# Kernel tuning notes

Measured on AMD Instinct MI355X. Metric: run time of the kernel, lower is better.

## Reference

```python
import jax, jax.numpy as jnp
import numpy as np

N_Q = 16
N_K = 16
D_QK = 64
D_V = 64
# torch module default scale=1.0 saturates softmax at feature width 1024;
# we use the conventional sqrt(d) scale for well-conditioned numerics.
SCALE = 32.0  # sqrt(N_Q * D_QK)
DROPOUT_P = 0.0  # dropout is identity at p=0


def setup_inputs() -> dict:
    key = jax.random.key(0)
    kq, kk, kv = jax.random.split(key, 3)
    S = 8192
    return {
        "query": jax.random.normal(kq, (S, N_Q, D_QK), dtype=jnp.float32),
        "key": jax.random.normal(kk, (S, N_K, D_QK), dtype=jnp.float32),
        "value": jax.random.normal(kv, (S, N_K, D_V), dtype=jnp.float32),
    }


def reference(query, key, value):
    # Flatten trailing (head, dim) into one feature axis, as the torch view does.
    q = query.reshape(-1, N_Q * D_QK)            # [S_q, 1024]
    k = key.reshape(-1, N_K * D_QK)              # [S_k, 1024]
    v = value.reshape(-1, N_K * D_V)             # [S_k, 1024]
    scores = jnp.matmul(q, k.T) / SCALE          # [S_q, S_k]
    attn = jax.nn.softmax(scores, axis=-1)       # dropout_p=0 -> identity
    out = jnp.matmul(attn, v)                    # [S_q, 1024]
    return out.reshape(query.shape[:-1] + (-1,))  # [S_q, N_Q, D_V]
```

## Files before the change

### kernel.cpp

```cpp
#include <hip/hip_runtime.h>
#include <hip/hip_bf16.h>


typedef __bf16 bf16x8 __attribute__((ext_vector_type(8)));
typedef float f32x4 __attribute__((ext_vector_type(4)));
typedef const __attribute__((address_space(1))) unsigned int* as1p;
typedef __attribute__((address_space(3))) unsigned int* as3p;
typedef unsigned short u16;

__device__ __forceinline__ u16 f2bf(float x) {
  unsigned u = __float_as_uint(x);
  u += 0x7fffu + ((u >> 16) & 1u);
  return (u16)(u >> 16);
}
__device__ __forceinline__ float bf2f(u16 b) { return __uint_as_float(((unsigned)b) << 16); }
__device__ __forceinline__ unsigned pack2(float lo, float hi) {
  return (unsigned)f2bf(lo) | ((unsigned)f2bf(hi) << 16);
}

#define BAR()   do { __builtin_amdgcn_s_barrier(); asm volatile("" ::: "memory"); } while (0)
#define LGKM0() do { asm volatile("s_waitcnt lgkmcnt(0)" ::: "memory"); __builtin_amdgcn_sched_barrier(0); } while (0)
#define VM(n)   do { asm volatile("s_waitcnt vmcnt(" #n ")" ::: "memory"); __builtin_amdgcn_sched_barrier(0); } while (0)

__global__ __launch_bounds__(256) void cvt_bf16(const float* __restrict__ in,
                                                unsigned short* __restrict__ out) {
  const size_t i = (size_t)blockIdx.x * 256 + threadIdx.x;
  const float4* p = (const float4*)in + i * 2;
  float4 a = p[0], b = p[1];
  uint4 o;
  o.x = pack2(a.x, a.y);
  o.y = pack2(a.z, a.w);
  o.z = pack2(b.x, b.y);
  o.w = pack2(b.z, b.w);
  ((uint4*)out)[i] = o;
}

__global__ __launch_bounds__(256) void transpose_bf16(const float* __restrict__ V,
                                                      unsigned short* __restrict__ VT) {
  __shared__ float t[64][65];
  const int rb = blockIdx.x * 64;
  const int cb = blockIdx.y * 64;
  const int tid = threadIdx.x;
#pragma unroll
  for (int it = 0; it < 4; ++it) {
    int r = it * 16 + (tid >> 4);
    int c = (tid & 15) * 4;
    float4 x = *(const float4*)(V + (size_t)(rb + r) * 1024 + cb + c);
    t[r][c] = x.x; t[r][c + 1] = x.y; t[r][c + 2] = x.z; t[r][c + 3] = x.w;
  }
  __syncthreads();
  const int j = tid & 63;
  const int c0 = (tid >> 6) * 16;
#pragma unroll
  for (int i = 0; i < 16; ++i) {
    int c = c0 + i;
    VT[(size_t)(cb + c) * 8192 + rb + j] = f2bf(t[j][c]);
  }
}

template <int BM, int OUTMODE, int DEC>
__global__ __launch_bounds__(512, 2) void gemm8(const u16* __restrict__ A,
                                                const u16* __restrict__ B,
                                                void* __restrict__ Cv,
                                                const float* __restrict__ inv,
                                                float* __restrict__ partials,
                                                int K, int ldc, float scale) {
  constexpr int MF = BM / 32;
  constexpr int MH = MF / 2;
  constexpr int LA = BM / 64;
  constexpr int NU = (LA + 4) / 2;
  constexpr int ABUF = BM * 128;
  constexpr int BBUF = 32768;
  constexpr int BUFSZ = ABUF + BBUF;
  static_assert(NU == 3 || NU == 4, "");
  __shared__ __align__(1024) char smem[2 * BUFSZ];

  const int tid = threadIdx.x;
  const int lane = tid & 63, wave = tid >> 6;
  const int wr = wave >> 2, wc = wave & 3;
  const int lan15 = lane & 15, g = lane >> 4, l7 = lane & 7;

  const int nwg = gridDim.x;
  const int wg = (blockIdx.x & 7) * (nwg >> 3) + (blockIdx.x >> 3);

  int bm0, bn0;
  if constexpr (DEC == 0) {
    const int r = wg & 255;
    bm0 = (r >> 3) * 256;
    bn0 = (((wg >> 8) << 3) | (r & 7)) * 256;
  } else {
    bm0 = (wg & 63) * BM;
    bn0 = (wg >> 6) * 256;
  }

  const int sr = tid >> 3;
  const int scb = ((tid & 7) ^ (sr & 7)) * 8;
  const u16* Ags = A + (size_t)(bm0 + sr) * K + scb;
  const u16* Bgs = B + (size_t)(bn0 + sr) * K + scb;

  const int sa0 = ((0 + g) ^ l7) * 16;
  const int sa1 = ((4 + g) ^ l7) * 16;
  const int abase = (wr * (BM / 2) + lan15) * 128;
  const int bbase = ABUF + (wc * 64 + lan15) * 128;

  f32x4 acc[MF][4];
#pragma unroll
  for (int m = 0; m < MF; ++m)
#pragma unroll
    for (int n = 0; n < 4; ++n) acc[m][n] = f32x4{0.f, 0.f, 0.f, 0.f};

  const int nt = K >> 6;
  const int niter = nt >> 1;

  auto ISSUE_UNIT = [&](int t, int u) {
    const int bb = (t & 1) * BUFSZ;
    const size_t ko = (size_t)t * 64;
    if (2 * u < LA) {
#pragma unroll
      for (int s = 0; s < 2; ++s) {
        const int j = 2 * u + s;
        __builtin_amdgcn_global_load_lds((as1p)(Ags + (size_t)j * 64 * K + ko),
                                         (as3p)(smem + bb + j * 8192 + tid * 16), 16, 0, 0);
      }
    } else {
#pragma unroll
      for (int s = 0; s < 2; ++s) {
        const int j = 2 * u - LA + s;
        __builtin_amdgcn_global_load_lds((as1p)(Bgs + (size_t)j * 64 * K + ko),
                                         (as3p)(smem + bb + ABUF + j * 8192 + tid * 16), 16, 0, 0);
      }
    }
  };

  bf16x8 a[MH][2], b[4][2];
  auto DS_A = [&](int bb, int mh) {
#pragma unroll
    for (int m = 0; m < MH; ++m) {
      a[m][0] = *(const bf16x8*)(smem + bb + abase + (mh * MH + m) * 2048 + sa0);
      a[m][1] = *(const bf16x8*)(smem + bb + abase + (mh * MH + m) * 2048 + sa1);
    }
  };
  auto DS_B = [&](int bb, int nh) {
#pragma unroll
    for (int n = 0; n < 2; ++n) {
      b[nh * 2 + n][0] = *(const bf16x8*)(smem + bb + bbase + (nh * 2 + n) * 2048 + sa0);
      b[nh * 2 + n][1] = *(const bf16x8*)(smem + bb + bbase + (nh * 2 + n) * 2048 + sa1);
    }
  };
  auto MMA = [&](int mh, int nh) {
    __builtin_amdgcn_s_setprio(1);
#pragma unroll
    for (int m = 0; m < MH; ++m)
#pragma unroll
      for (int n = 0; n < 2; ++n)
#pragma unroll
        for (int ks = 0; ks < 2; ++ks)
          acc[mh * MH + m][nh * 2 + n] = __builtin_amdgcn_mfma_f32_16x16x32_bf16(
              a[m][ks], b[nh * 2 + n][ks], acc[mh * MH + m][nh * 2 + n], 0, 0, 0);
    __builtin_amdgcn_s_setprio(0);
  };

#pragma unroll
  for (int u = 0; u < NU; ++u) ISSUE_UNIT(0, u);
  ISSUE_UNIT(1, 0);
  VM(2);
  BAR();

  for (int i = 0; i < niter; ++i) {
    const int t0 = 2 * i;
    const bool more = (i + 1 < niter);

    DS_A(0, 0); DS_B(0, 0);
    ISSUE_UNIT(t0 + 1, 1);
    BAR(); MMA(0, 0); BAR();

    DS_B(0, 1);
    if constexpr (NU >= 3) ISSUE_UNIT(t0 + 1, 2);
    BAR(); MMA(0, 1); BAR();

    DS_A(0, 1);
    if constexpr (NU >= 4) ISSUE_UNIT(t0 + 1, 3);
    BAR(); MMA(1, 0); LGKM0(); BAR();

    if (more) ISSUE_UNIT(t0 + 2, 0);
    BAR(); MMA(1, 1);
    if (more) { VM(2); } else { VM(0); }
    BAR();

    DS_A(BUFSZ, 0); DS_B(BUFSZ, 0);
    if (more) ISSUE_UNIT(t0 + 2, 1);
    BAR(); MMA(0, 0); BAR();

    DS_B(BUFSZ, 1);
    if (more) { if constexpr (NU >= 3) ISSUE_UNIT(t0 + 2, 2); }
    BAR(); MMA(0, 1); BAR();

    DS_A(BUFSZ, 1);
    if (more) { if constexpr (NU >= 4) ISSUE_UNIT(t0 + 2, 3); }
    BAR(); MMA(1, 0); LGKM0(); BAR();

    if (more) ISSUE_UNIT(t0 + 3, 0);
    BAR(); MMA(1, 1);
    if (more) { VM(2); } else { VM(0); }
    BAR();
  }

  const int c0 = bn0 + wc * 64 + lan15;
  if constexpr (OUTMODE == 0) {
    u16* C = (u16*)Cv;
    const int cb4 = (bn0 >> 8) * 4 + wc;
#pragma unroll
    for (int m = 0; m < MF; ++m)
#pragma unroll
      for (int r = 0; r < 4; ++r) {
        const int row = bm0 + wr * (BM / 2) + m * 16 + g * 4 + r;
        float part = 0.f;
#pragma unroll
        for (int n = 0; n < 4; ++n) {
          float v = __expf(acc[m][n][r] * scale);
          C[(size_t)row * ldc + c0 + n * 16] = f2bf(v);
          part += v;
        }
        part += __shfl_xor(part, 1, 64);
        part += __shfl_xor(part, 2, 64);
        part += __shfl_xor(part, 4, 64);
        part += __shfl_xor(part, 8, 64);
        if (lan15 == 0) partials[(size_t)row * 128 + cb4] = part;
      }
  } else {
    float* C = (float*)Cv;
#pragma unroll
    for (int m = 0; m < MF; ++m)
#pragma unroll
      for (int r = 0; r < 4; ++r) {
        const int row = bm0 + wr * (BM / 2) + m * 16 + g * 4 + r;
        const float iv = inv ? inv[row] : 1.0f;
#pragma unroll
        for (int n = 0; n < 4; ++n)
          C[(size_t)row * ldc + c0 + n * 16] = acc[m][n][r] * iv;
      }
  }
}

__global__ __launch_bounds__(256) void rowinv(const float* __restrict__ partials,
                                              float* __restrict__ inv) {
  const int row = blockIdx.x * 256 + threadIdx.x;
  const float4* p = (const float4*)(partials + (size_t)row * 128);
  float s = 0.f;
#pragma unroll
  for (int j = 0; j < 32; ++j) {
    float4 v = p[j];
    s += (v.x + v.y) + (v.z + v.w);
  }
  inv[row] = 1.0f / s;
}

__global__ __launch_bounds__(256) void normalize_inplace(u16* __restrict__ E) {
  __shared__ float red[4];
  u16* row = E + (size_t)blockIdx.x * 8192;
  const int tid = threadIdx.x;
  float f[32];
  float s = 0.f;
#pragma unroll
  for (int c = 0; c < 4; ++c) {
    uint4 v = *((const uint4*)row + c * 256 + tid);
    unsigned u[4] = {v.x, v.y, v.z, v.w};
#pragma unroll
    for (int q = 0; q < 4; ++q) {
      f[c * 8 + q * 2] = bf2f((u16)(u[q] & 0xffffu));
      f[c * 8 + q * 2 + 1] = bf2f((u16)(u[q] >> 16));
      s += f[c * 8 + q * 2] + f[c * 8 + q * 2 + 1];
    }
  }
#pragma unroll
  for (int off = 32; off; off >>= 1) s += __shfl_xor(s, off, 64);
  if ((tid & 63) == 0) red[tid >> 6] = s;
  __syncthreads();
  const float iv = 1.0f / ((red[0] + red[1]) + (red[2] + red[3]));
#pragma unroll
  for (int c = 0; c < 4; ++c) {
    uint4 o;
    o.x = pack2(f[c * 8 + 0] * iv, f[c * 8 + 1] * iv);
    o.y = pack2(f[c * 8 + 2] * iv, f[c * 8 + 3] * iv);
    o.z = pack2(f[c * 8 + 4] * iv, f[c * 8 + 5] * iv);
    o.w = pack2(f[c * 8 + 6] * iv, f[c * 8 + 7] * iv);
    *((uint4*)row + c * 256 + tid) = o;
  }
}

extern "C" void kernel_launch(void* const* d_in, const int* in_sizes, int n_in,
                              void* d_out, int out_size, void* d_ws, size_t ws_size,
                              hipStream_t stream) {
  const float* Q = (const float*)d_in[0];
  const float* K = (const float*)d_in[1];
  const float* V = (const float*)d_in[2];

  char* ws = (char*)d_ws;
  u16* S = (u16*)ws;
  u16* VT = (u16*)(ws + (size_t)134217728);
  float* partials = (float*)(ws + (size_t)134217728 + 16777216);
  float* inv = (float*)(ws + (size_t)134217728 + 16777216 + 4194304);
  const bool haveInv =
      ws_size >= (size_t)134217728 + 16777216 + 4194304 + 32768;

  u16* Qb = (u16*)d_out;
  u16* Kb = Qb + 8388608;

  cvt_bf16<<<4096, 256, 0, stream>>>(Q, Qb);
  cvt_bf16<<<4096, 256, 0, stream>>>(K, Kb);
  transpose_bf16<<<dim3(128, 16), 256, 0, stream>>>(V, VT);

  gemm8<256, 0, 0><<<1024, 512, 0, stream>>>(
      Qb, Kb, S, nullptr, haveInv ? partials : (float*)(ws + 134217728 + 16777216),
      1024, 8192, 1.0f / 32.0f);

  if (haveInv) {
    rowinv<<<32, 256, 0, stream>>>(partials, inv);
    gemm8<128, 1, 1><<<256, 512, 0, stream>>>(
        S, VT, d_out, inv, nullptr, 8192, 1024, 1.0f);
  } else {
    normalize_inplace<<<8192, 256, 0, stream>>>(S);
    gemm8<128, 1, 1><<<256, 512, 0, stream>>>(
        S, VT, d_out, nullptr, nullptr, 8192, 1024, 1.0f);
  }
}
```

Before: 305.6 us.

## Replace 8-phase interleaved GEMM schedule with simple per-tile double-buffered loop

The main loop of both GEMM kernels changes from an 8-phase schedule that interleaved LDS reads, split global-to-LDS load units and MFMA groups with many barriers into a simpler loop. Each K-tile now loads all A/B fragments, runs all MFMAs, syncs once, then issues the whole tile two ahead. This removes most barriers and the fine-grained load splitting. In exchange the LDS-read latency is no longer hidden behind MFMA work, and more fragments are held in registers at once, which raises register pressure.

```diff
diff --git a/kernel.cpp b/kernel.cpp
--- a/kernel.cpp
+++ b/kernel.cpp
@@ -59,20 +59,20 @@
 }
 
 template <int BM, int OUTMODE, int DEC>
-__global__ __launch_bounds__(512, 2) void gemm8(const u16* __restrict__ A,
-                                                const u16* __restrict__ B,
-                                                void* __restrict__ Cv,
-                                                const float* __restrict__ inv,
-                                                float* __restrict__ partials,
-                                                int K, int ldc, float scale) {
+__global__ __launch_bounds__(512, 2) void gemm_fr(const u16* __restrict__ A,
+                                                  const u16* __restrict__ B,
+                                                  void* __restrict__ Cv,
+                                                  const float* __restrict__ inv,
+                                                  float* __restrict__ partials,
+                                                  int K, int ldc, float scale) {
   constexpr int MF = BM / 32;
   constexpr int MH = MF / 2;
   constexpr int LA = BM / 64;
-  constexpr int NU = (LA + 4) / 2;
+  constexpr int LB = 4;
+  constexpr int LPT = LA + LB;
   constexpr int ABUF = BM * 128;
   constexpr int BBUF = 32768;
   constexpr int BUFSZ = ABUF + BBUF;
-  static_assert(NU == 3 || NU == 4, "");
   __shared__ __align__(1024) char smem[2 * BUFSZ];
 
   const int tid = threadIdx.x;
@@ -110,98 +110,88 @@
     for (int n = 0; n < 4; ++n) acc[m][n] = f32x4{0.f, 0.f, 0.f, 0.f};
 
   const int nt = K >> 6;
-  const int niter = nt >> 1;
-
-  auto ISSUE_UNIT = [&](int t, int u) {
+
+  auto ISSUE = [&](int t) {
     const int bb = (t & 1) * BUFSZ;
     const size_t ko = (size_t)t * 64;
-    if (2 * u < LA) {
-#pragma unroll
-      for (int s = 0; s < 2; ++s) {
-        const int j = 2 * u + s;
-        __builtin_amdgcn_global_load_lds((as1p)(Ags + (size_t)j * 64 * K + ko),
-                                         (as3p)(smem + bb + j * 8192 + tid * 16), 16, 0, 0);
+#pragma unroll
+    for (int j = 0; j < LA; ++j)
+      __builtin_amdgcn_global_load_lds((as1p)(Ags + (size_t)j * 64 * K + ko),
+                                       (as3p)(smem + bb + j * 8192 + tid * 16), 16, 0, 0);
+#pragma unroll
+    for (int j = 0; j < LB; ++j)
+      __builtin_amdgcn_global_load_lds((as1p)(Bgs + (size_t)j * 64 * K + ko),
+                                       (as3p)(smem + bb + ABUF + j * 8192 + tid * 16), 16, 0, 0);
+  };
+
+  ISSUE(0);
+  ISSUE(1);
+  if constexpr (LPT == 8) { VM(8); } else { VM(6); }
+  BAR();
+
+  for (int t = 0; t < nt; ++t) {
+    const char* bp = smem + (t & 1) * BUFSZ;
+
+    bf16x8 a0[MH][2], b0[4][2], a1[MH][2];
+#pragma unroll
+    for (int m = 0; m < MH; ++m) {
+      a0[m][0] = *(const bf16x8*)(bp + abase + m * 2048 + sa0);
+      a0[m][1] = *(const bf16x8*)(bp + abase + m * 2048 + sa1);
+    }
+#pragma unroll
+    for (int n = 0; n < 4; ++n) {
+      b0[n][0] = *(const bf16x8*)(bp + bbase + n * 2048 + sa0);
+      b0[n][1] = *(const bf16x8*)(bp + bbase + n * 2048 + sa1);
+    }
+#pragma unroll
+    for (int m = 0; m < MH; ++m) {
+      a1[m][0] = *(const bf16x8*)(bp + abase + (MH + m) * 2048 + sa0);
+      a1[m][1] = *(const bf16x8*)(bp + abase + (MH + m) * 2048 + sa1);
+    }
+
+    __builtin_amdgcn_s_setprio(1);
+#pragma unroll
+    for (int m = 0; m < MH; ++m)
+#pragma unroll
+      for (int n = 0; n < 2; ++n)
+#pragma unroll
+        for (int ks = 0; ks < 2; ++ks)
+          acc[m][n] = __builtin_amdgcn_mfma_f32_16x16x32_bf16(a0[m][ks], b0[n][ks], acc[m][n], 0, 0, 0);
+#pragma unroll
+    for (int m = 0; m < MH; ++m)
+#pragma unroll
+      for (int n = 0; n < 2; ++n)
+#pragma unroll
+        for (int ks = 0; ks < 2; ++ks)
+          acc[m][2 + n] = __builtin_amdgcn_mfma_f32_16x16x32_bf16(a0[m][ks], b0[2 + n][ks], acc[m][2 + n], 0, 0, 0);
+#pragma unroll
+    for (int m = 0; m < MH; ++m)
+#pragma unroll
+      for (int n = 0; n < 2; ++n)
+#pragma unroll
+        for (int ks = 0; ks < 2; ++ks)
+          acc[MH + m][n] = __builtin_amdgcn_mfma_f32_16x16x32_bf16(a1[m][ks], b0[n][ks], acc[MH + m][n], 0, 0, 0);
+#pragma unroll
+    for (int m = 0; m < MH; ++m)
+#pragma unroll
+      for (int n = 0; n < 2; ++n)
+#pragma unroll
+        for (int ks = 0; ks < 2; ++ks)
+          acc[MH + m][2 + n] = __builtin_amdgcn_mfma_f32_16x16x32_bf16(a1[m][ks], b0[2 + n][ks], acc[MH + m][2 + n], 0, 0, 0);
+    __builtin_amdgcn_s_setprio(0);
+
+    LGKM0();
+    BAR();
+
+    const bool st = (t + 2 < nt);
+    if (st) ISSUE(t + 2);
+    if (t + 1 < nt) {
+      if (st) {
+        if constexpr (LPT == 8) { VM(8); } else { VM(6); }
+      } else {
+        VM(0);
       }
-    } else {
-#pragma unroll
-      for (int s = 0; s < 2; ++s) {
-        const int j = 2 * u - LA + s;
-        __builtin_amdgcn_global_load_lds((as1p)(Bgs + (size_t)j * 64 * K + ko),
-                                         (as3p)(smem + bb + ABUF + j * 8192 + tid * 16), 16, 0, 0);
-      }
-    }
-  };
-
-  bf16x8 a[MH][2], b[4][2];
-  auto DS_A = [&](int bb, int mh) {
-#pragma unroll
-    for (int m = 0; m < MH; ++m) {
-      a[m][0] = *(const bf16x8*)(smem + bb + abase + (mh * MH + m) * 2048 + sa0);
-      a[m][1] = *(const bf16x8*)(smem + bb + abase + (mh * MH + m) * 2048 + sa1);
-    }
-  };
-  auto DS_B = [&](int bb, int nh) {
-#pragma unroll
-    for (int n = 0; n < 2; ++n) {
-      b[nh * 2 + n][0] = *(const bf16x8*)(smem + bb + bbase + (nh * 2 + n) * 2048 + sa0);
-      b[nh * 2 + n][1] = *(const bf16x8*)(smem + bb + bbase + (nh * 2 + n) * 2048 + sa1);
-    }
-  };
-  auto MMA = [&](int mh, int nh) {
-    __builtin_amdgcn_s_setprio(1);
-#pragma unroll
-    for (int m = 0; m < MH; ++m)
-#pragma unroll
-      for (int n = 0; n < 2; ++n)
-#pragma unroll
-        for (int ks = 0; ks < 2; ++ks)
-          acc[mh * MH + m][nh * 2 + n] = __builtin_amdgcn_mfma_f32_16x16x32_bf16(
-              a[m][ks], b[nh * 2 + n][ks], acc[mh * MH + m][nh * 2 + n], 0, 0, 0);
-    __builtin_amdgcn_s_setprio(0);
-  };
-
-#pragma unroll
-  for (int u = 0; u < NU; ++u) ISSUE_UNIT(0, u);
-  ISSUE_UNIT(1, 0);
-  VM(2);
-  BAR();
-
-  for (int i = 0; i < niter; ++i) {
-    const int t0 = 2 * i;
-    const bool more = (i + 1 < niter);
-
-    DS_A(0, 0); DS_B(0, 0);
-    ISSUE_UNIT(t0 + 1, 1);
-    BAR(); MMA(0, 0); BAR();
-
-    DS_B(0, 1);
-    if constexpr (NU >= 3) ISSUE_UNIT(t0 + 1, 2);
-    BAR(); MMA(0, 1); BAR();
-
-    DS_A(0, 1);
-    if constexpr (NU >= 4) ISSUE_UNIT(t0 + 1, 3);
-    BAR(); MMA(1, 0); LGKM0(); BAR();
-
-    if (more) ISSUE_UNIT(t0 + 2, 0);
-    BAR(); MMA(1, 1);
-    if (more) { VM(2); } else { VM(0); }
-    BAR();
-
-    DS_A(BUFSZ, 0); DS_B(BUFSZ, 0);
-    if (more) ISSUE_UNIT(t0 + 2, 1);
-    BAR(); MMA(0, 0); BAR();
-
-    DS_B(BUFSZ, 1);
-    if (more) { if constexpr (NU >= 3) ISSUE_UNIT(t0 + 2, 2); }
-    BAR(); MMA(0, 1); BAR();
-
-    DS_A(BUFSZ, 1);
-    if (more) { if constexpr (NU >= 4) ISSUE_UNIT(t0 + 2, 3); }
-    BAR(); MMA(1, 0); LGKM0(); BAR();
-
-    if (more) ISSUE_UNIT(t0 + 3, 0);
-    BAR(); MMA(1, 1);
-    if (more) { VM(2); } else { VM(0); }
+    }
     BAR();
   }
 
@@ -310,17 +300,17 @@
   cvt_bf16<<<4096, 256, 0, stream>>>(K, Kb);
   transpose_bf16<<<dim3(128, 16), 256, 0, stream>>>(V, VT);
 
-  gemm8<256, 0, 0><<<1024, 512, 0, stream>>>(
+  gemm_fr<256, 0, 0><<<1024, 512, 0, stream>>>(
       Qb, Kb, S, nullptr, haveInv ? partials : (float*)(ws + 134217728 + 16777216),
       1024, 8192, 1.0f / 32.0f);
 
   if (haveInv) {
     rowinv<<<32, 256, 0, stream>>>(partials, inv);
-    gemm8<128, 1, 1><<<256, 512, 0, stream>>>(
+    gemm_fr<128, 1, 1><<<256, 512, 0, stream>>>(
         S, VT, d_out, inv, nullptr, 8192, 1024, 1.0f);
   } else {
     normalize_inplace<<<8192, 256, 0, stream>>>(S);
-    gemm8<128, 1, 1><<<256, 512, 0, stream>>>(
+    gemm_fr<128, 1, 1><<<256, 512, 0, stream>>>(
         S, VT, d_out, nullptr, nullptr, 8192, 1024, 1.0f);
   }
 }
```

New measurement: 320.7 us. 4.9% more time.

## Reorder GEMM prefetch schedule for deeper lookahead and remap second-GEMM tile order

Applied to the files above, without the earlier changes.

Global-to-LDS loads are now issued at a finer granularity and in a new order. Each half of the next A/B tiles is prefetched as soon as the matching LDS sub-buffer has been read, which deepens the outstanding loads (vmcnt 6 or 4 instead of 2). LDS-read waits are placed before each MMA phase rather than only before the third. Separately, the second GEMM's workgroup-to-tile mapping groups 8 M-blocks by all 4 N-blocks, so neighbouring blocks share S rows and VT columns in cache. The risks are buffer-reuse hazards from the earlier overwrites and extra lgkm stalls.

```diff
diff --git a/kernel.cpp b/kernel.cpp
--- a/kernel.cpp
+++ b/kernel.cpp
@@ -59,20 +59,17 @@
 }
 
 template <int BM, int OUTMODE, int DEC>
-__global__ __launch_bounds__(512, 2) void gemm8(const u16* __restrict__ A,
-                                                const u16* __restrict__ B,
-                                                void* __restrict__ Cv,
-                                                const float* __restrict__ inv,
-                                                float* __restrict__ partials,
-                                                int K, int ldc, float scale) {
+__global__ __launch_bounds__(512, 2) void gemm8d(const u16* __restrict__ A,
+                                                 const u16* __restrict__ B,
+                                                 void* __restrict__ Cv,
+                                                 const float* __restrict__ inv,
+                                                 float* __restrict__ partials,
+                                                 int K, int ldc, float scale) {
   constexpr int MF = BM / 32;
   constexpr int MH = MF / 2;
-  constexpr int LA = BM / 64;
-  constexpr int NU = (LA + 4) / 2;
   constexpr int ABUF = BM * 128;
   constexpr int BBUF = 32768;
   constexpr int BUFSZ = ABUF + BBUF;
-  static_assert(NU == 3 || NU == 4, "");
   __shared__ __align__(1024) char smem[2 * BUFSZ];
 
   const int tid = threadIdx.x;
@@ -82,15 +79,16 @@
 
   const int nwg = gridDim.x;
   const int wg = (blockIdx.x & 7) * (nwg >> 3) + (blockIdx.x >> 3);
-
   int bm0, bn0;
   if constexpr (DEC == 0) {
     const int r = wg & 255;
     bm0 = (r >> 3) * 256;
     bn0 = (((wg >> 8) << 3) | (r & 7)) * 256;
   } else {
-    bm0 = (wg & 63) * BM;
-    bn0 = (wg >> 6) * 256;
+    const int chunk = wg >> 5;
+    const int within = wg & 31;
+    bm0 = (chunk * 8 + (within >> 2)) * BM;
+    bn0 = (within & 3) * 256;
   }
 
   const int sr = tid >> 3;
@@ -112,25 +110,24 @@
   const int nt = K >> 6;
   const int niter = nt >> 1;
 
-  auto ISSUE_UNIT = [&](int t, int u) {
-    const int bb = (t & 1) * BUFSZ;
+  auto IA = [&](int t, int ja, int jb) {
+    char* bb = smem + (t & 1) * BUFSZ;
     const size_t ko = (size_t)t * 64;
-    if (2 * u < LA) {
-#pragma unroll
-      for (int s = 0; s < 2; ++s) {
-        const int j = 2 * u + s;
-        __builtin_amdgcn_global_load_lds((as1p)(Ags + (size_t)j * 64 * K + ko),
-                                         (as3p)(smem + bb + j * 8192 + tid * 16), 16, 0, 0);
-      }
-    } else {
-#pragma unroll
-      for (int s = 0; s < 2; ++s) {
-        const int j = 2 * u - LA + s;
-        __builtin_amdgcn_global_load_lds((as1p)(Bgs + (size_t)j * 64 * K + ko),
-                                         (as3p)(smem + bb + ABUF + j * 8192 + tid * 16), 16, 0, 0);
-      }
-    }
-  };
+    __builtin_amdgcn_global_load_lds((as1p)(Ags + (size_t)ja * 64 * K + ko),
+                                     (as3p)(bb + ja * 8192 + tid * 16), 16, 0, 0);
+    __builtin_amdgcn_global_load_lds((as1p)(Ags + (size_t)jb * 64 * K + ko),
+                                     (as3p)(bb + jb * 8192 + tid * 16), 16, 0, 0);
+  };
+  auto IB = [&](int t, int j0) {
+    char* bb = smem + (t & 1) * BUFSZ + ABUF;
+    const size_t ko = (size_t)t * 64;
+    __builtin_amdgcn_global_load_lds((as1p)(Bgs + (size_t)j0 * 64 * K + ko),
+                                     (as3p)(bb + j0 * 8192 + tid * 16), 16, 0, 0);
+    __builtin_amdgcn_global_load_lds((as1p)(Bgs + (size_t)(j0 + 1) * 64 * K + ko),
+                                     (as3p)(bb + (j0 + 1) * 8192 + tid * 16), 16, 0, 0);
+  };
+  auto IA_mh0 = [&](int t) { if constexpr (BM == 256) IA(t, 0, 2); };
+  auto IA_mh1 = [&](int t) { if constexpr (BM == 256) IA(t, 1, 3); else IA(t, 0, 1); };
 
   bf16x8 a[MH][2], b[4][2];
   auto DS_A = [&](int bb, int mh) {
@@ -160,10 +157,15 @@
     __builtin_amdgcn_s_setprio(0);
   };
 
-#pragma unroll
-  for (int u = 0; u < NU; ++u) ISSUE_UNIT(0, u);
-  ISSUE_UNIT(1, 0);
-  VM(2);
+  if constexpr (BM == 256) {
+    IA(0, 0, 2); IB(0, 0); IB(0, 2); IA(0, 1, 3);
+    IA(1, 0, 2); IB(1, 0); IB(1, 2);
+    VM(6);
+  } else {
+    IB(0, 0); IB(0, 2); IA(0, 0, 1);
+    IB(1, 0); IB(1, 2);
+    VM(4);
+  }
   BAR();
 
   for (int i = 0; i < niter; ++i) {
@@ -171,37 +173,37 @@
     const bool more = (i + 1 < niter);
 
     DS_A(0, 0); DS_B(0, 0);
-    ISSUE_UNIT(t0 + 1, 1);
-    BAR(); MMA(0, 0); BAR();
+    IA_mh1(t0 + 1);
+    BAR(); LGKM0(); MMA(0, 0); BAR();
 
     DS_B(0, 1);
-    if constexpr (NU >= 3) ISSUE_UNIT(t0 + 1, 2);
-    BAR(); MMA(0, 1); BAR();
+    if (more) IA_mh0(t0 + 2);
+    BAR(); LGKM0(); MMA(0, 1); BAR();
 
     DS_A(0, 1);
-    if constexpr (NU >= 4) ISSUE_UNIT(t0 + 1, 3);
-    BAR(); MMA(1, 0); LGKM0(); BAR();
-
-    if (more) ISSUE_UNIT(t0 + 2, 0);
+    if (more) IB(t0 + 2, 0);
+    BAR(); LGKM0(); MMA(1, 0); BAR();
+
+    if (more) IB(t0 + 2, 2);
     BAR(); MMA(1, 1);
-    if (more) { VM(2); } else { VM(0); }
+    if (more) { if constexpr (BM == 256) VM(6); else VM(4); } else { VM(0); }
     BAR();
 
     DS_A(BUFSZ, 0); DS_B(BUFSZ, 0);
-    if (more) ISSUE_UNIT(t0 + 2, 1);
-    BAR(); MMA(0, 0); BAR();
+    if (more) IA_mh1(t0 + 2);
+    BAR(); LGKM0(); MMA(0, 0); BAR();
 
     DS_B(BUFSZ, 1);
-    if (more) { if constexpr (NU >= 3) ISSUE_UNIT(t0 + 2, 2); }
-    BAR(); MMA(0, 1); BAR();
+    if (more) IA_mh0(t0 + 3);
+    BAR(); LGKM0(); MMA(0, 1); BAR();
 
     DS_A(BUFSZ, 1);
-    if (more) { if constexpr (NU >= 4) ISSUE_UNIT(t0 + 2, 3); }
-    BAR(); MMA(1, 0); LGKM0(); BAR();
-
-    if (more) ISSUE_UNIT(t0 + 3, 0);
+    if (more) IB(t0 + 3, 0);
+    BAR(); LGKM0(); MMA(1, 0); BAR();
+
+    if (more) IB(t0 + 3, 2);
     BAR(); MMA(1, 1);
-    if (more) { VM(2); } else { VM(0); }
+    if (more) { if constexpr (BM == 256) VM(6); else VM(4); } else { VM(0); }
     BAR();
   }
 
@@ -310,17 +312,17 @@
   cvt_bf16<<<4096, 256, 0, stream>>>(K, Kb);
   transpose_bf16<<<dim3(128, 16), 256, 0, stream>>>(V, VT);
 
-  gemm8<256, 0, 0><<<1024, 512, 0, stream>>>(
+  gemm8d<256, 0, 0><<<1024, 512, 0, stream>>>(
       Qb, Kb, S, nullptr, haveInv ? partials : (float*)(ws + 134217728 + 16777216),
       1024, 8192, 1.0f / 32.0f);
 
   if (haveInv) {
     rowinv<<<32, 256, 0, stream>>>(partials, inv);
-    gemm8<128, 1, 1><<<256, 512, 0, stream>>>(
+    gemm8d<128, 1, 1><<<256, 512, 0, stream>>>(
         S, VT, d_out, inv, nullptr, 8192, 1024, 1.0f);
   } else {
     normalize_inplace<<<8192, 256, 0, stream>>>(S);
-    gemm8<128, 1, 1><<<256, 512, 0, stream>>>(
+    gemm8d<128, 1, 1><<<256, 512, 0, stream>>>(
         S, VT, d_out, nullptr, nullptr, 8192, 1024, 1.0f);
   }
 }
```

Result: no change. 304.3 us (-0.4%).
